# Performance work log

Hardware: AMD Instinct MI355X
Metric: run time of the kernel (lower is better)

Reference implementation:

```python
import jax, jax.numpy as jnp
import numpy as np

B, T, C = 2, 2048, 2048
H, D = 16, 128
ROPE_THETA = 100000.0


def _rms_norm(x):
    eps = jnp.asarray(jnp.finfo(x.dtype).eps, x.dtype)
    var = jnp.mean(jnp.square(x), axis=-1, keepdims=True)
    return x * jax.lax.rsqrt(var + eps)


def _apply_rotary(x, cos, sin):
    # x: [B,T,H,D]; cos/sin: [T,1,D//2] broadcasting over (B, H)
    d = x.shape[-1] // 2
    x1, x2 = x[..., :d], x[..., d:]
    y1 = x1 * cos + x2 * sin
    y2 = -x1 * sin + x2 * cos
    return jnp.concatenate([y1, y2], axis=-1)


def setup_inputs() -> dict:
    key = jax.random.key(0)
    ks = jax.random.split(key, 5)
    x = jax.random.normal(ks[0], (B, T, C), dtype=jnp.float32)
    # rotary table (caller-provided, already offset-applied)
    inv_freq = 1.0 / (ROPE_THETA ** (np.arange(0, D // 2, dtype=np.float32) / (D // 2)))
    t = np.arange(T, dtype=np.float32)
    freqs = np.outer(t, inv_freq)  # [T, D//2]
    cos = jnp.asarray(np.cos(freqs))[:, None, :]  # [T,1,D//2]
    sin = jnp.asarray(np.sin(freqs))[:, None, :]
    std = 0.02
    Wq = jax.random.normal(ks[1], (C, C), dtype=jnp.float32) * std
    Wk = jax.random.normal(ks[2], (C, C), dtype=jnp.float32) * std
    Wv = jax.random.normal(ks[3], (C, C), dtype=jnp.float32) * std
    Wo = jax.random.normal(ks[4], (C, C), dtype=jnp.float32) * std
    return {"x": x, "cos": cos, "sin": sin, "Wq": Wq, "Wk": Wk, "Wv": Wv, "Wo": Wo}


def reference(x, cos, sin, Wq, Wk, Wv, Wo):
    b, t, _ = x.shape
    # torch Linear: y = x @ W.T
    q = (x @ Wq.T).reshape(b, t, H, D)
    k = (x @ Wk.T).reshape(b, t, H, D)
    v = (x @ Wv.T).reshape(b, t, H, D)
    # qk RMSNorm (qk_norm=True)
    q = _rms_norm(q)
    k = _rms_norm(k)
    # rotary
    q = _apply_rotary(q, cos, sin)
    k = _apply_rotary(k, cos, sin)
    # causal SDPA, scale = 1/sqrt(D)
    scale = 1.0 / jnp.sqrt(jnp.asarray(D, x.dtype))
    scores = jnp.einsum('bthd,bshd->bhts', q, k) * scale  # [B,H,T,T]
    causal = jnp.tril(jnp.ones((t, t), dtype=bool))
    scores = jnp.where(causal[None, None], scores, jnp.asarray(-jnp.inf, x.dtype))
    attn = jax.nn.softmax(scores, axis=-1)
    o = jnp.einsum('bhts,bshd->bthd', attn, v).reshape(b, t, H * D)
    return o @ Wo.T
```

## Files before the change

kernel.cpp:

```cpp
#include <hip/hip_runtime.h>

using u16 = unsigned short;
typedef __attribute__((ext_vector_type(8))) short short8;
typedef __attribute__((ext_vector_type(4))) float f32x4;

#define DEV __device__ __forceinline__

DEV float bf2f(u16 u) { union { unsigned i; float f; } v; v.i = (unsigned)u << 16; return v.f; }
DEV u16 f2bf(float f) {
  union { float f; unsigned i; } v; v.f = f;
  return (u16)((v.i + 0x7fffu + ((v.i >> 16) & 1u)) >> 16);
}
DEV void async16(void* lds, const void* g) {
  __builtin_amdgcn_global_load_lds((const __attribute__((address_space(1))) void*)g,
                                   (__attribute__((address_space(3))) void*)lds, 16, 0, 0);
}

__global__ __launch_bounds__(256) void cvt_bf16(const float* __restrict__ in,
                                                u16* __restrict__ out, int n) {
  int i = (blockIdx.x * 256 + threadIdx.x) * 8;
  if (i >= n) return;
  const float4* p = (const float4*)(in + i);
  float4 a = p[0], b = p[1];
  short8 o;
  o[0] = (short)f2bf(a.x); o[1] = (short)f2bf(a.y);
  o[2] = (short)f2bf(a.z); o[3] = (short)f2bf(a.w);
  o[4] = (short)f2bf(b.x); o[5] = (short)f2bf(b.y);
  o[6] = (short)f2bf(b.z); o[7] = (short)f2bf(b.w);
  *(short8*)(out + i) = o;
}

template <bool BF16OUT>
DEV void gemm_body(const u16* __restrict__ A, const u16* __restrict__ Bw,
                   void* __restrict__ C, u16* As, u16* Bs) {
  constexpr int KD = 2048, N = 2048;
  const int tid = threadIdx.x, lane = tid & 63, w = tid >> 6;
  const int wm = (w >> 1) * 64, wn = (w & 1) * 64;
  const int lr = lane & 15, lk = lane >> 4;
  const size_t m0 = (size_t)blockIdx.y * 128, n0 = (size_t)blockIdx.x * 128;

  f32x4 acc[4][4];
#pragma unroll
  for (int i = 0; i < 4; ++i)
#pragma unroll
    for (int j = 0; j < 4; ++j) acc[i][j] = (f32x4){0.f, 0.f, 0.f, 0.f};

  const int bo0 = tid * 16;
  for (int kt = 0; kt < KD; kt += 32) {
#pragma unroll
    for (int i = 0; i < 2; ++i) {
      int bo = i * 4096 + bo0;
      int row = bo >> 6, cb = bo & 63;
      async16((char*)As + i * 4096 + w * 1024,
              (const char*)A + ((m0 + row) * KD + kt) * 2 + cb);
    }
#pragma unroll
    for (int i = 0; i < 2; ++i) {
      int bo = i * 4096 + bo0;
      int row = bo >> 6, cb = bo & 63;
      async16((char*)Bs + i * 4096 + w * 1024,
              (const char*)Bw + ((n0 + row) * KD + kt) * 2 + cb);
    }
    __syncthreads();
    short8 a[4], b[4];
#pragma unroll
    for (int mi = 0; mi < 4; ++mi)
      a[mi] = *(const short8*)(As + (wm + mi * 16 + lr) * 32 + lk * 8);
#pragma unroll
    for (int ni = 0; ni < 4; ++ni)
      b[ni] = *(const short8*)(Bs + (wn + ni * 16 + lr) * 32 + lk * 8);
#pragma unroll
    for (int mi = 0; mi < 4; ++mi)
#pragma unroll
      for (int ni = 0; ni < 4; ++ni)
        acc[mi][ni] =
            __builtin_amdgcn_mfma_f32_16x16x32_bf16(a[mi], b[ni], acc[mi][ni], 0, 0, 0);
    __syncthreads();
  }
#pragma unroll
  for (int mi = 0; mi < 4; ++mi)
#pragma unroll
    for (int ni = 0; ni < 4; ++ni)
#pragma unroll
      for (int r = 0; r < 4; ++r) {
        size_t row = m0 + wm + mi * 16 + lk * 4 + r;
        size_t col = n0 + wn + ni * 16 + lr;
        if constexpr (BF16OUT)
          ((u16*)C)[row * N + col] = f2bf(acc[mi][ni][r]);
        else
          ((float*)C)[row * N + col] = acc[mi][ni][r];
      }
}

__global__ __launch_bounds__(256) void gemm_qkv(
    const u16* __restrict__ X, const u16* __restrict__ Wq, const u16* __restrict__ Wk,
    const u16* __restrict__ Wv, u16* __restrict__ Qo, u16* __restrict__ Ko,
    u16* __restrict__ Vo) {
  __shared__ u16 As[128 * 32], Bs[128 * 32];
  const u16* W = blockIdx.z == 0 ? Wq : (blockIdx.z == 1 ? Wk : Wv);
  u16* C = blockIdx.z == 0 ? Qo : (blockIdx.z == 1 ? Ko : Vo);
  gemm_body<true>(X, W, C, As, Bs);
}

__global__ __launch_bounds__(256) void gemm_out(const u16* __restrict__ A,
                                                const u16* __restrict__ W,
                                                float* __restrict__ C) {
  __shared__ u16 As[128 * 32], Bs[128 * 32];
  gemm_body<false>(A, W, C, As, Bs);
}

__global__ __launch_bounds__(256) void rmsrope(u16* __restrict__ q, u16* __restrict__ k,
                                               const float* __restrict__ cosb,
                                               const float* __restrict__ sinb) {
  int gw = blockIdx.x * 4 + (threadIdx.x >> 6);
  int lane = threadIdx.x & 63;
  u16* base = q;
  float pre = 0.088388347648318447f * 1.4426950408889634f;
  if (gw >= 65536) { base = k; gw -= 65536; pre = 1.0f; }
  int bt = gw >> 4, h = gw & 15, t = bt & 2047;
  u16* p = base + (size_t)bt * 2048 + h * 128;
  float x1 = bf2f(p[lane]), x2 = bf2f(p[lane + 64]);
  float ss = x1 * x1 + x2 * x2;
#pragma unroll
  for (int m = 1; m < 64; m <<= 1) ss += __shfl_xor(ss, m, 64);
  float rn = rsqrtf(ss * (1.0f / 128.0f) + 1.1920929e-7f) * pre;
  float c = cosb[t * 64 + lane], s = sinb[t * 64 + lane];
  float y1 = (x1 * c + x2 * s) * rn;
  float y2 = (x2 * c - x1 * s) * rn;
  p[lane] = f2bf(y1);
  p[lane + 64] = f2bf(y2);
}

__global__ __launch_bounds__(256) void transpose_v(const u16* __restrict__ v,
                                                   u16* __restrict__ vt) {
  __shared__ u16 tile[64][72];
  int bh = blockIdx.z, b = bh >> 4, h = bh & 15;
  int t0 = blockIdx.x * 64, d0 = blockIdx.y * 64;
  int tid = threadIdx.x;
  int rr = tid >> 3, ch = tid & 7;
#pragma unroll
  for (int p = 0; p < 2; ++p) {
    int t = rr + p * 32;
    const u16* src = v + ((size_t)(b * 2048 + t0 + t) * 2048 + h * 128 + d0 + ch * 8);
    *(short8*)&tile[t][ch * 8] = *(const short8*)src;
  }
  __syncthreads();
#pragma unroll
  for (int p = 0; p < 2; ++p) {
    int d = rr + p * 32;
    int oc = ch * 8;
    short8 val;
#pragma unroll
    for (int j = 0; j < 8; ++j) val[j] = (short)tile[oc + j][d];
    *(short8*)(vt + ((size_t)(bh * 128 + d0 + d) * 2048 + t0 + oc)) = val;
  }
}

__global__ __launch_bounds__(256) void attn_fwd(const u16* __restrict__ Q,
                                                const u16* __restrict__ K,
                                                const u16* __restrict__ Vt,
                                                u16* __restrict__ O) {
  __shared__ u16 Ks[128 * 128];
  __shared__ u16 Vs[128 * 128];
  __shared__ u16 Ps[4][16 * 128];
  const int tid = threadIdx.x, lane = tid & 63, w = tid >> 6;
  const int lr = lane & 15, lk = lane >> 4;
  const int bh = blockIdx.y, b = bh >> 4, h = bh & 15;

  const char* kbase = (const char*)(K + ((size_t)b * 2048) * 2048 + h * 128);
  const char* vbase = (const char*)(Vt + (size_t)bh * 128 * 2048);
  const int bo0 = tid * 16;
  u16* pw = Ps[w];

  for (int qi = 0; qi < 2; ++qi) {
    const int qt = qi ? (31 - (int)blockIdx.x) : (int)blockIdx.x;
    const int qw = qt * 64 + w * 16;
    const int nt = (qt >> 1) + 1;
    const int nlim = (qt & 1) ? 8 : 4;

    short8 aq[4];
    const u16* qptr = Q + ((size_t)(b * 2048 + qw + lr)) * 2048 + h * 128;
#pragma unroll
    for (int kk = 0; kk < 4; ++kk) aq[kk] = *(const short8*)(qptr + kk * 32 + lk * 8);

    float mrow[4], lrow[4];
    f32x4 o[8];
#pragma unroll
    for (int r = 0; r < 4; ++r) { mrow[r] = -__builtin_inff(); lrow[r] = 0.f; }
#pragma unroll
    for (int nd = 0; nd < 8; ++nd) o[nd] = (f32x4){0.f, 0.f, 0.f, 0.f};

    for (int kt = 0; kt < nt; ++kt) {
      const int kv0 = kt * 128;
      const bool diag = (kt == nt - 1);
#pragma unroll
      for (int i = 0; i < 8; ++i) {
        int bo = i * 4096 + bo0;
        int r = bo >> 8, cb = bo & 255;
        async16((char*)Ks + i * 4096 + w * 1024,
                kbase + (size_t)(kv0 + r) * 4096 + (cb ^ ((r & 7) << 4)));
      }
#pragma unroll
      for (int i = 0; i < 8; ++i) {
        int bo = i * 4096 + bo0;
        int d = bo >> 8, cb = bo & 255;
        async16((char*)Vs + i * 4096 + w * 1024,
                vbase + (size_t)d * 4096 + (size_t)kv0 * 2 + (cb ^ ((d & 7) << 4)));
      }
      __syncthreads();

      f32x4 s[8];
#pragma unroll
      for (int n = 0; n < 8; ++n) {
        s[n] = (f32x4){-__builtin_inff(), -__builtin_inff(), -__builtin_inff(),
                       -__builtin_inff()};
        if (!diag || n < nlim) {
          f32x4 t = (f32x4){0.f, 0.f, 0.f, 0.f};
#pragma unroll
          for (int kk = 0; kk < 4; ++kk) {
            int row = n * 16 + lr;
            int cb = kk * 64 + lk * 16;
            short8 bk =
                *(const short8*)((const char*)Ks + row * 256 + (cb ^ ((row & 7) << 4)));
            t = __builtin_amdgcn_mfma_f32_16x16x32_bf16(aq[kk], bk, t, 0, 0, 0);
          }
          s[n] = t;
        }
      }
      if (diag) {
#pragma unroll
        for (int n = 0; n < 8; ++n)
#pragma unroll
          for (int r = 0; r < 4; ++r) {
            int col = kv0 + n * 16 + lr;
            int row = qw + lk * 4 + r;
            if (col > row) s[n][r] = -__builtin_inff();
          }
      }
      float al[4];
#pragma unroll
      for (int r = 0; r < 4; ++r) {
        float mx = s[0][r];
#pragma unroll
        for (int n = 1; n < 8; ++n) mx = fmaxf(mx, s[n][r]);
        mx = fmaxf(mx, __shfl_xor(mx, 1, 64));
        mx = fmaxf(mx, __shfl_xor(mx, 2, 64));
        mx = fmaxf(mx, __shfl_xor(mx, 4, 64));
        mx = fmaxf(mx, __shfl_xor(mx, 8, 64));
        float mn = fmaxf(mrow[r], mx);
        al[r] = exp2f(mrow[r] - mn);
        mrow[r] = mn;
      }
      float rs[4] = {0.f, 0.f, 0.f, 0.f};
#pragma unroll
      for (int n = 0; n < 8; ++n)
#pragma unroll
        for (int r = 0; r < 4; ++r) {
          float pv = exp2f(s[n][r] - mrow[r]);
          s[n][r] = pv;
          rs[r] += pv;
        }
#pragma unroll
      for (int r = 0; r < 4; ++r) {
        float t = rs[r];
        t += __shfl_xor(t, 1, 64); t += __shfl_xor(t, 2, 64);
        t += __shfl_xor(t, 4, 64); t += __shfl_xor(t, 8, 64);
        lrow[r] = lrow[r] * al[r] + t;
      }
#pragma unroll
      for (int nd = 0; nd < 8; ++nd)
#pragma unroll
        for (int r = 0; r < 4; ++r) o[nd][r] *= al[r];

#pragma unroll
      for (int n = 0; n < 8; ++n)
#pragma unroll
        for (int r = 0; r < 4; ++r) {
          int prow = lk * 4 + r;
          pw[prow * 128 + ((n * 16 + lr) ^ ((prow & 7) << 3))] = f2bf(s[n][r]);
        }

#pragma unroll
      for (int kk = 0; kk < 4; ++kk) {
        short8 pa = *(const short8*)(pw + lr * 128 + ((kk * 32 + lk * 8) ^ ((lr & 7) << 3)));
#pragma unroll
        for (int nd = 0; nd < 8; ++nd) {
          int dr = nd * 16 + lr;
          int cb = kk * 64 + lk * 16;
          short8 bv =
              *(const short8*)((const char*)Vs + dr * 256 + (cb ^ ((dr & 7) << 4)));
          o[nd] = __builtin_amdgcn_mfma_f32_16x16x32_bf16(pa, bv, o[nd], 0, 0, 0);
        }
      }
      __syncthreads();
    }

    u16* op = O + ((size_t)(b * 2048 + qw + lk * 4)) * 2048 + h * 128;
#pragma unroll
    for (int r = 0; r < 4; ++r) {
      float inv = 1.0f / lrow[r];
#pragma unroll
      for (int nd = 0; nd < 8; ++nd)
        op[(size_t)r * 2048 + nd * 16 + lr] = f2bf(o[nd][r] * inv);
    }
  }
}

extern "C" void kernel_launch(void* const* d_in, const int* in_sizes, int n_in,
                              void* d_out, int out_size, void* d_ws, size_t ws_size,
                              hipStream_t stream) {
  const float* x = (const float*)d_in[0];
  const float* cosb = (const float*)d_in[1];
  const float* sinb = (const float*)d_in[2];
  const float* Wq = (const float*)d_in[3];
  const float* Wk = (const float*)d_in[4];
  const float* Wv = (const float*)d_in[5];
  const float* Wo = (const float*)d_in[6];
  float* out = (float*)d_out;
  char* ws = (char*)d_ws;

  const size_t XB = (size_t)4096 * 2048 * 2;
  const size_t WB = (size_t)2048 * 2048 * 2;
  u16* xb  = (u16*)(ws);
  u16* wqb = (u16*)(ws + XB);
  u16* wkb = (u16*)(ws + XB + WB);
  u16* wvb = (u16*)(ws + XB + 2 * WB);
  u16* wob = (u16*)(ws + XB + 3 * WB);
  u16* qb  = (u16*)(ws + XB + 4 * WB);
  u16* kb  = (u16*)(ws + XB + 4 * WB + XB);
  u16* vb  = (u16*)(ws + XB + 4 * WB + 2 * XB);
  u16* vtb = (u16*)(ws + XB + 4 * WB + 3 * XB);
  u16* ob  = (u16*)(ws + XB + 4 * WB + 4 * XB);

  cvt_bf16<<<4096, 256, 0, stream>>>(x, xb, 8388608);
  cvt_bf16<<<2048, 256, 0, stream>>>(Wq, wqb, 4194304);
  cvt_bf16<<<2048, 256, 0, stream>>>(Wk, wkb, 4194304);
  cvt_bf16<<<2048, 256, 0, stream>>>(Wv, wvb, 4194304);
  cvt_bf16<<<2048, 256, 0, stream>>>(Wo, wob, 4194304);
  gemm_qkv<<<dim3(16, 32, 3), 256, 0, stream>>>(xb, wqb, wkb, wvb, qb, kb, vb);
  rmsrope<<<32768, 256, 0, stream>>>(qb, kb, cosb, sinb);
  transpose_v<<<dim3(32, 2, 32), 256, 0, stream>>>(vb, vtb);
  attn_fwd<<<dim3(16, 32), 256, 0, stream>>>(qb, kb, vtb, ob);
  gemm_out<<<dim3(16, 32), 256, 0, stream>>>(ob, wob, out);
}
```

Measured before the change: 477.4 us.

## Share K/V tiles between paired far and near query tiles in attention

Each attention block now processes its far and near causal query tiles together in one KV loop instead of two sequential passes. Every loaded K/V tile is used by both query tiles, so the near tile's KV loads are no longer issued separately. The grid is reordered so heads map to blockIdx.x, and launch_bounds gains a minimum of 2 blocks per CU. The cost is twice the accumulator and Q register state per thread, which raises register pressure and may cause spills under the occupancy bound.

```diff
diff --git a/kernel.cpp b/kernel.cpp
--- a/kernel.cpp
+++ b/kernel.cpp
@@ -156,152 +156,174 @@
   }
 }
 
-__global__ __launch_bounds__(256) void attn_fwd(const u16* __restrict__ Q,
-                                                const u16* __restrict__ K,
-                                                const u16* __restrict__ Vt,
-                                                u16* __restrict__ O) {
+DEV void attn_step(const short8* aq, float* mrow, float* lrow, f32x4* o,
+                   const u16* Ks, const u16* Vs, u16* pw,
+                   int lr, int lk, bool diag, int nlim, int qw, int kv0) {
+  f32x4 s[8];
+#pragma unroll
+  for (int n = 0; n < 8; ++n) {
+    s[n] = (f32x4){-__builtin_inff(), -__builtin_inff(), -__builtin_inff(),
+                   -__builtin_inff()};
+    if (!diag || n < nlim) {
+      f32x4 t = (f32x4){0.f, 0.f, 0.f, 0.f};
+#pragma unroll
+      for (int kk = 0; kk < 4; ++kk) {
+        int row = n * 16 + lr;
+        int cb = kk * 64 + lk * 16;
+        short8 bk =
+            *(const short8*)((const char*)Ks + row * 256 + (cb ^ ((row & 7) << 4)));
+        t = __builtin_amdgcn_mfma_f32_16x16x32_bf16(aq[kk], bk, t, 0, 0, 0);
+      }
+      s[n] = t;
+    }
+  }
+  if (diag) {
+#pragma unroll
+    for (int n = 0; n < 8; ++n)
+#pragma unroll
+      for (int r = 0; r < 4; ++r) {
+        int col = kv0 + n * 16 + lr;
+        int row = qw + lk * 4 + r;
+        if (col > row) s[n][r] = -__builtin_inff();
+      }
+  }
+  float al[4];
+#pragma unroll
+  for (int r = 0; r < 4; ++r) {
+    float mx = s[0][r];
+#pragma unroll
+    for (int n = 1; n < 8; ++n) mx = fmaxf(mx, s[n][r]);
+    mx = fmaxf(mx, __shfl_xor(mx, 1, 64));
+    mx = fmaxf(mx, __shfl_xor(mx, 2, 64));
+    mx = fmaxf(mx, __shfl_xor(mx, 4, 64));
+    mx = fmaxf(mx, __shfl_xor(mx, 8, 64));
+    float mn = fmaxf(mrow[r], mx);
+    al[r] = exp2f(mrow[r] - mn);
+    mrow[r] = mn;
+  }
+  float rs[4] = {0.f, 0.f, 0.f, 0.f};
+#pragma unroll
+  for (int n = 0; n < 8; ++n)
+#pragma unroll
+    for (int r = 0; r < 4; ++r) {
+      float pv = exp2f(s[n][r] - mrow[r]);
+      s[n][r] = pv;
+      rs[r] += pv;
+    }
+#pragma unroll
+  for (int r = 0; r < 4; ++r) {
+    float t = rs[r];
+    t += __shfl_xor(t, 1, 64); t += __shfl_xor(t, 2, 64);
+    t += __shfl_xor(t, 4, 64); t += __shfl_xor(t, 8, 64);
+    lrow[r] = lrow[r] * al[r] + t;
+  }
+#pragma unroll
+  for (int nd = 0; nd < 8; ++nd)
+#pragma unroll
+    for (int r = 0; r < 4; ++r) o[nd][r] *= al[r];
+
+#pragma unroll
+  for (int n = 0; n < 8; ++n)
+#pragma unroll
+    for (int r = 0; r < 4; ++r) {
+      int prow = lk * 4 + r;
+      pw[prow * 128 + ((n * 16 + lr) ^ ((prow & 7) << 3))] = f2bf(s[n][r]);
+    }
+
+#pragma unroll
+  for (int kk = 0; kk < 4; ++kk) {
+    short8 pa = *(const short8*)(pw + lr * 128 + ((kk * 32 + lk * 8) ^ ((lr & 7) << 3)));
+#pragma unroll
+    for (int nd = 0; nd < 8; ++nd) {
+      int dr = nd * 16 + lr;
+      int cb = kk * 64 + lk * 16;
+      short8 bv = *(const short8*)((const char*)Vs + dr * 256 + (cb ^ ((dr & 7) << 4)));
+      o[nd] = __builtin_amdgcn_mfma_f32_16x16x32_bf16(pa, bv, o[nd], 0, 0, 0);
+    }
+  }
+}
+
+__global__ __launch_bounds__(256, 2) void attn_fwd(const u16* __restrict__ Q,
+                                                   const u16* __restrict__ K,
+                                                   const u16* __restrict__ Vt,
+                                                   u16* __restrict__ O) {
   __shared__ u16 Ks[128 * 128];
   __shared__ u16 Vs[128 * 128];
   __shared__ u16 Ps[4][16 * 128];
   const int tid = threadIdx.x, lane = tid & 63, w = tid >> 6;
   const int lr = lane & 15, lk = lane >> 4;
-  const int bh = blockIdx.y, b = bh >> 4, h = bh & 15;
+  const int bh = blockIdx.x, b = bh >> 4, h = bh & 15;
+  const int p = blockIdx.y;
+
+  const int qt_f = 31 - p, qt_n = p;
+  const int qw_f = qt_f * 64 + w * 16, qw_n = qt_n * 64 + w * 16;
+  const int nt_f = (qt_f >> 1) + 1, nt_n = (qt_n >> 1) + 1;
+  const int nlim_f = (qt_f & 1) ? 8 : 4, nlim_n = (qt_n & 1) ? 8 : 4;
 
   const char* kbase = (const char*)(K + ((size_t)b * 2048) * 2048 + h * 128);
   const char* vbase = (const char*)(Vt + (size_t)bh * 128 * 2048);
   const int bo0 = tid * 16;
   u16* pw = Ps[w];
 
-  for (int qi = 0; qi < 2; ++qi) {
-    const int qt = qi ? (31 - (int)blockIdx.x) : (int)blockIdx.x;
-    const int qw = qt * 64 + w * 16;
-    const int nt = (qt >> 1) + 1;
-    const int nlim = (qt & 1) ? 8 : 4;
-
-    short8 aq[4];
-    const u16* qptr = Q + ((size_t)(b * 2048 + qw + lr)) * 2048 + h * 128;
-#pragma unroll
-    for (int kk = 0; kk < 4; ++kk) aq[kk] = *(const short8*)(qptr + kk * 32 + lk * 8);
-
-    float mrow[4], lrow[4];
-    f32x4 o[8];
-#pragma unroll
-    for (int r = 0; r < 4; ++r) { mrow[r] = -__builtin_inff(); lrow[r] = 0.f; }
-#pragma unroll
-    for (int nd = 0; nd < 8; ++nd) o[nd] = (f32x4){0.f, 0.f, 0.f, 0.f};
-
-    for (int kt = 0; kt < nt; ++kt) {
-      const int kv0 = kt * 128;
-      const bool diag = (kt == nt - 1);
-#pragma unroll
-      for (int i = 0; i < 8; ++i) {
-        int bo = i * 4096 + bo0;
-        int r = bo >> 8, cb = bo & 255;
-        async16((char*)Ks + i * 4096 + w * 1024,
-                kbase + (size_t)(kv0 + r) * 4096 + (cb ^ ((r & 7) << 4)));
-      }
-#pragma unroll
-      for (int i = 0; i < 8; ++i) {
-        int bo = i * 4096 + bo0;
-        int d = bo >> 8, cb = bo & 255;
-        async16((char*)Vs + i * 4096 + w * 1024,
-                vbase + (size_t)d * 4096 + (size_t)kv0 * 2 + (cb ^ ((d & 7) << 4)));
-      }
-      __syncthreads();
-
-      f32x4 s[8];
-#pragma unroll
-      for (int n = 0; n < 8; ++n) {
-        s[n] = (f32x4){-__builtin_inff(), -__builtin_inff(), -__builtin_inff(),
-                       -__builtin_inff()};
-        if (!diag || n < nlim) {
-          f32x4 t = (f32x4){0.f, 0.f, 0.f, 0.f};
-#pragma unroll
-          for (int kk = 0; kk < 4; ++kk) {
-            int row = n * 16 + lr;
-            int cb = kk * 64 + lk * 16;
-            short8 bk =
-                *(const short8*)((const char*)Ks + row * 256 + (cb ^ ((row & 7) << 4)));
-            t = __builtin_amdgcn_mfma_f32_16x16x32_bf16(aq[kk], bk, t, 0, 0, 0);
-          }
-          s[n] = t;
-        }
-      }
-      if (diag) {
-#pragma unroll
-        for (int n = 0; n < 8; ++n)
-#pragma unroll
-          for (int r = 0; r < 4; ++r) {
-            int col = kv0 + n * 16 + lr;
-            int row = qw + lk * 4 + r;
-            if (col > row) s[n][r] = -__builtin_inff();
-          }
-      }
-      float al[4];
-#pragma unroll
-      for (int r = 0; r < 4; ++r) {
-        float mx = s[0][r];
-#pragma unroll
-        for (int n = 1; n < 8; ++n) mx = fmaxf(mx, s[n][r]);
-        mx = fmaxf(mx, __shfl_xor(mx, 1, 64));
-        mx = fmaxf(mx, __shfl_xor(mx, 2, 64));
-        mx = fmaxf(mx, __shfl_xor(mx, 4, 64));
-        mx = fmaxf(mx, __shfl_xor(mx, 8, 64));
-        float mn = fmaxf(mrow[r], mx);
-        al[r] = exp2f(mrow[r] - mn);
-        mrow[r] = mn;
-      }
-      float rs[4] = {0.f, 0.f, 0.f, 0.f};
-#pragma unroll
-      for (int n = 0; n < 8; ++n)
-#pragma unroll
-        for (int r = 0; r < 4; ++r) {
-          float pv = exp2f(s[n][r] - mrow[r]);
-          s[n][r] = pv;
-          rs[r] += pv;
-        }
-#pragma unroll
-      for (int r = 0; r < 4; ++r) {
-        float t = rs[r];
-        t += __shfl_xor(t, 1, 64); t += __shfl_xor(t, 2, 64);
-        t += __shfl_xor(t, 4, 64); t += __shfl_xor(t, 8, 64);
-        lrow[r] = lrow[r] * al[r] + t;
-      }
-#pragma unroll
-      for (int nd = 0; nd < 8; ++nd)
-#pragma unroll
-        for (int r = 0; r < 4; ++r) o[nd][r] *= al[r];
-
-#pragma unroll
-      for (int n = 0; n < 8; ++n)
-#pragma unroll
-        for (int r = 0; r < 4; ++r) {
-          int prow = lk * 4 + r;
-          pw[prow * 128 + ((n * 16 + lr) ^ ((prow & 7) << 3))] = f2bf(s[n][r]);
-        }
-
-#pragma unroll
-      for (int kk = 0; kk < 4; ++kk) {
-        short8 pa = *(const short8*)(pw + lr * 128 + ((kk * 32 + lk * 8) ^ ((lr & 7) << 3)));
-#pragma unroll
-        for (int nd = 0; nd < 8; ++nd) {
-          int dr = nd * 16 + lr;
-          int cb = kk * 64 + lk * 16;
-          short8 bv =
-              *(const short8*)((const char*)Vs + dr * 256 + (cb ^ ((dr & 7) << 4)));
-          o[nd] = __builtin_amdgcn_mfma_f32_16x16x32_bf16(pa, bv, o[nd], 0, 0, 0);
-        }
-      }
-      __syncthreads();
-    }
-
-    u16* op = O + ((size_t)(b * 2048 + qw + lk * 4)) * 2048 + h * 128;
-#pragma unroll
-    for (int r = 0; r < 4; ++r) {
-      float inv = 1.0f / lrow[r];
-#pragma unroll
-      for (int nd = 0; nd < 8; ++nd)
-        op[(size_t)r * 2048 + nd * 16 + lr] = f2bf(o[nd][r] * inv);
+  short8 aq_f[4], aq_n[4];
+  {
+    const u16* qf = Q + ((size_t)(b * 2048 + qw_f + lr)) * 2048 + h * 128;
+    const u16* qn = Q + ((size_t)(b * 2048 + qw_n + lr)) * 2048 + h * 128;
+#pragma unroll
+    for (int kk = 0; kk < 4; ++kk) {
+      aq_f[kk] = *(const short8*)(qf + kk * 32 + lk * 8);
+      aq_n[kk] = *(const short8*)(qn + kk * 32 + lk * 8);
+    }
+  }
+
+  float m_f[4], l_f[4], m_n[4], l_n[4];
+  f32x4 o_f[8], o_n[8];
+#pragma unroll
+  for (int r = 0; r < 4; ++r) {
+    m_f[r] = -__builtin_inff(); l_f[r] = 0.f;
+    m_n[r] = -__builtin_inff(); l_n[r] = 0.f;
+  }
+#pragma unroll
+  for (int nd = 0; nd < 8; ++nd) {
+    o_f[nd] = (f32x4){0.f, 0.f, 0.f, 0.f};
+    o_n[nd] = (f32x4){0.f, 0.f, 0.f, 0.f};
+  }
+
+  for (int kt = 0; kt < nt_f; ++kt) {
+    const int kv0 = kt * 128;
+#pragma unroll
+    for (int i = 0; i < 8; ++i) {
+      int bo = i * 4096 + bo0;
+      int r = bo >> 8, cb = bo & 255;
+      async16((char*)Ks + i * 4096 + w * 1024,
+              kbase + (size_t)(kv0 + r) * 4096 + (cb ^ ((r & 7) << 4)));
+    }
+#pragma unroll
+    for (int i = 0; i < 8; ++i) {
+      int bo = i * 4096 + bo0;
+      int d = bo >> 8, cb = bo & 255;
+      async16((char*)Vs + i * 4096 + w * 1024,
+              vbase + (size_t)d * 4096 + (size_t)kv0 * 2 + (cb ^ ((d & 7) << 4)));
+    }
+    __syncthreads();
+
+    attn_step(aq_f, m_f, l_f, o_f, Ks, Vs, pw, lr, lk, kt == nt_f - 1, nlim_f,
+              qw_f, kv0);
+    if (kt < nt_n)
+      attn_step(aq_n, m_n, l_n, o_n, Ks, Vs, pw, lr, lk, kt == nt_n - 1, nlim_n,
+                qw_n, kv0);
+    __syncthreads();
+  }
+
+  u16* of = O + ((size_t)(b * 2048 + qw_f + lk * 4)) * 2048 + h * 128;
+  u16* on = O + ((size_t)(b * 2048 + qw_n + lk * 4)) * 2048 + h * 128;
+#pragma unroll
+  for (int r = 0; r < 4; ++r) {
+    float invf = 1.0f / l_f[r], invn = 1.0f / l_n[r];
+#pragma unroll
+    for (int nd = 0; nd < 8; ++nd) {
+      of[(size_t)r * 2048 + nd * 16 + lr] = f2bf(o_f[nd][r] * invf);
+      on[(size_t)r * 2048 + nd * 16 + lr] = f2bf(o_n[nd][r] * invn);
     }
   }
 }
@@ -340,6 +362,6 @@
   gemm_qkv<<<dim3(16, 32, 3), 256, 0, stream>>>(xb, wqb, wkb, wvb, qb, kb, vb);
   rmsrope<<<32768, 256, 0, stream>>>(qb, kb, cosb, sinb);
   transpose_v<<<dim3(32, 2, 32), 256, 0, stream>>>(vb, vtb);
-  attn_fwd<<<dim3(16, 32), 256, 0, stream>>>(qb, kb, vtb, ob);
+  attn_fwd<<<dim3(32, 16), 256, 0, stream>>>(qb, kb, vtb, ob);
   gemm_out<<<dim3(16, 32), 256, 0, stream>>>(ob, wob, out);
 }
```

Result: slower. 719.4 us (+50.7%).

## Double-buffer K/V tiles in attention and swap grid axes for head-major scheduling

Applied to the files above, without the earlier changes.

The attention kernel now keeps two LDS buffers for K and V. It prefetches the next KV tile asynchronously while computing on the current one, using explicit vmcnt waits and barriers in place of the load-then-sync pattern. The launch grid swaps its axes so consecutive blocks cover different batch-heads rather than different query tiles, which changes the dispatch order and L2 locality. LDS use doubles to roughly 144 KB per block, which limits occupancy to one block per CU.

```diff
diff --git a/kernel.cpp b/kernel.cpp
--- a/kernel.cpp
+++ b/kernel.cpp
@@ -160,20 +160,38 @@
                                                 const u16* __restrict__ K,
                                                 const u16* __restrict__ Vt,
                                                 u16* __restrict__ O) {
-  __shared__ u16 Ks[128 * 128];
-  __shared__ u16 Vs[128 * 128];
+  __shared__ u16 Ks[2][128 * 128];
+  __shared__ u16 Vs[2][128 * 128];
   __shared__ u16 Ps[4][16 * 128];
   const int tid = threadIdx.x, lane = tid & 63, w = tid >> 6;
   const int lr = lane & 15, lk = lane >> 4;
-  const int bh = blockIdx.y, b = bh >> 4, h = bh & 15;
+  const int bh = blockIdx.x, b = bh >> 4, h = bh & 15;
+  const int p = blockIdx.y;
 
   const char* kbase = (const char*)(K + ((size_t)b * 2048) * 2048 + h * 128);
   const char* vbase = (const char*)(Vt + (size_t)bh * 128 * 2048);
   const int bo0 = tid * 16;
   u16* pw = Ps[w];
 
+#define STAGE(KT, BUF)                                                              \
+  {                                                                                 \
+    const int kv0s = (KT)*128;                                                      \
+    _Pragma("unroll") for (int i = 0; i < 8; ++i) {                                 \
+      int bo = i * 4096 + bo0;                                                      \
+      int r = bo >> 8, cb = bo & 255;                                               \
+      async16((char*)Ks[BUF] + i * 4096 + w * 1024,                                 \
+              kbase + (size_t)(kv0s + r) * 4096 + (cb ^ ((r & 7) << 4)));           \
+    }                                                                               \
+    _Pragma("unroll") for (int i = 0; i < 8; ++i) {                                 \
+      int bo = i * 4096 + bo0;                                                      \
+      int d = bo >> 8, cb = bo & 255;                                               \
+      async16((char*)Vs[BUF] + i * 4096 + w * 1024,                                 \
+              vbase + (size_t)d * 4096 + (size_t)kv0s * 2 + (cb ^ ((d & 7) << 4))); \
+    }                                                                               \
+  }
+
   for (int qi = 0; qi < 2; ++qi) {
-    const int qt = qi ? (31 - (int)blockIdx.x) : (int)blockIdx.x;
+    const int qt = qi ? (31 - p) : p;
     const int qw = qt * 64 + w * 16;
     const int nt = (qt >> 1) + 1;
     const int nlim = (qt & 1) ? 8 : 4;
@@ -190,24 +208,26 @@
 #pragma unroll
     for (int nd = 0; nd < 8; ++nd) o[nd] = (f32x4){0.f, 0.f, 0.f, 0.f};
 
+    __builtin_amdgcn_s_barrier();
+    STAGE(0, 0);
+
     for (int kt = 0; kt < nt; ++kt) {
+      const int cur = kt & 1;
       const int kv0 = kt * 128;
       const bool diag = (kt == nt - 1);
-#pragma unroll
-      for (int i = 0; i < 8; ++i) {
-        int bo = i * 4096 + bo0;
-        int r = bo >> 8, cb = bo & 255;
-        async16((char*)Ks + i * 4096 + w * 1024,
-                kbase + (size_t)(kv0 + r) * 4096 + (cb ^ ((r & 7) << 4)));
-      }
-#pragma unroll
-      for (int i = 0; i < 8; ++i) {
-        int bo = i * 4096 + bo0;
-        int d = bo >> 8, cb = bo & 255;
-        async16((char*)Vs + i * 4096 + w * 1024,
-                vbase + (size_t)d * 4096 + (size_t)kv0 * 2 + (cb ^ ((d & 7) << 4)));
-      }
-      __syncthreads();
+
+      __builtin_amdgcn_s_barrier();
+      if (kt + 1 < nt) {
+        STAGE(kt + 1, cur ^ 1);
+        asm volatile("s_waitcnt vmcnt(16)" ::: "memory");
+      } else {
+        asm volatile("s_waitcnt vmcnt(0)" ::: "memory");
+      }
+      __builtin_amdgcn_s_barrier();
+      __builtin_amdgcn_sched_barrier(0);
+
+      const u16* Kc = Ks[cur];
+      const u16* Vc = Vs[cur];
 
       f32x4 s[8];
 #pragma unroll
@@ -221,7 +241,7 @@
             int row = n * 16 + lr;
             int cb = kk * 64 + lk * 16;
             short8 bk =
-                *(const short8*)((const char*)Ks + row * 256 + (cb ^ ((row & 7) << 4)));
+                *(const short8*)((const char*)Kc + row * 256 + (cb ^ ((row & 7) << 4)));
             t = __builtin_amdgcn_mfma_f32_16x16x32_bf16(aq[kk], bk, t, 0, 0, 0);
           }
           s[n] = t;
@@ -282,17 +302,17 @@
 
 #pragma unroll
       for (int kk = 0; kk < 4; ++kk) {
-        short8 pa = *(const short8*)(pw + lr * 128 + ((kk * 32 + lk * 8) ^ ((lr & 7) << 3)));
+        short8 pa =
+            *(const short8*)(pw + lr * 128 + ((kk * 32 + lk * 8) ^ ((lr & 7) << 3)));
 #pragma unroll
         for (int nd = 0; nd < 8; ++nd) {
           int dr = nd * 16 + lr;
           int cb = kk * 64 + lk * 16;
           short8 bv =
-              *(const short8*)((const char*)Vs + dr * 256 + (cb ^ ((dr & 7) << 4)));
+              *(const short8*)((const char*)Vc + dr * 256 + (cb ^ ((dr & 7) << 4)));
           o[nd] = __builtin_amdgcn_mfma_f32_16x16x32_bf16(pa, bv, o[nd], 0, 0, 0);
         }
       }
-      __syncthreads();
     }
 
     u16* op = O + ((size_t)(b * 2048 + qw + lk * 4)) * 2048 + h * 128;
@@ -304,6 +324,7 @@
         op[(size_t)r * 2048 + nd * 16 + lr] = f2bf(o[nd][r] * inv);
     }
   }
+#undef STAGE
 }
 
 extern "C" void kernel_launch(void* const* d_in, const int* in_sizes, int n_in,
@@ -340,6 +361,6 @@
   gemm_qkv<<<dim3(16, 32, 3), 256, 0, stream>>>(xb, wqb, wkb, wvb, qb, kb, vb);
   rmsrope<<<32768, 256, 0, stream>>>(qb, kb, cosb, sinb);
   transpose_v<<<dim3(32, 2, 32), 256, 0, stream>>>(vb, vtb);
-  attn_fwd<<<dim3(16, 32), 256, 0, stream>>>(qb, kb, vtb, ob);
+  attn_fwd<<<dim3(32, 16), 256, 0, stream>>>(qb, kb, vtb, ob);
   gemm_out<<<dim3(16, 32), 256, 0, stream>>>(ob, wob, out);
 }
```

Measured after the change: 465.4 us. -2.5%, faster.
